# Performance work log

Measured on AMD Instinct MI355X. Metric: run time of the kernel, lower is better.

## Reference

```python
import jax, jax.numpy as jnp
import numpy as np
import math

B, C, F, W = 2, 8, 512, 1024
HEADS = 8


def _mcl(x, Wm, b):
    # per-channel linear over feature dim: x (b,c,g,w), Wm (c,f,g), b (c,f)
    return jnp.einsum('bcgw,cfg->bcfw', x, Wm) + b[None, :, :, None]


def _conv(x, w, b, pad):
    y = jax.lax.conv_general_dilated(
        x, w, window_strides=(1, 1), padding=[(0, 0), (pad, pad)],
        dimension_numbers=('NCHW', 'OIHW', 'NCHW'))
    return y + b[None, :, None, None]


def _rope(t):
    # t: (..., seq, d); lucidrains-style interleaved rotary
    d = t.shape[-1]
    seq = t.shape[-2]
    inv_freq = 1.0 / (10000.0 ** (jnp.arange(0, d, 2, dtype=jnp.float32) / d))
    freqs = jnp.arange(seq, dtype=jnp.float32)[:, None] * inv_freq[None, :]  # (seq, d/2)
    emb = jnp.repeat(freqs, 2, axis=-1)  # (seq, d), interleaved f0,f0,f1,f1,...
    cos, sin = jnp.cos(emb), jnp.sin(emb)
    tp = t.reshape(t.shape[:-1] + (d // 2, 2))
    rot = jnp.stack([-tp[..., 1], tp[..., 0]], axis=-1).reshape(t.shape)
    return t * cos.astype(t.dtype) + rot * sin.astype(t.dtype)


def setup_inputs() -> dict:
    key = jax.random.key(0)
    ks = jax.random.split(key, 18)
    s = 0.02
    d = {'x': jax.random.normal(ks[0], (B, C, F, W), dtype=jnp.float32)}
    names = ['q', 'k', 'v', 'o']
    for i, n in enumerate(names):
        d['W' + n] = jax.random.normal(ks[1 + 4 * i], (C, F, F), dtype=jnp.float32) * s
        d['b' + n] = jnp.zeros((C, F), dtype=jnp.float32)
        kw = 7 if n != 'o' else 1
        d[n + '_conv_w'] = jax.random.normal(ks[2 + 4 * i], (C, C, 1, kw), dtype=jnp.float32) * s
        d[n + '_conv_b'] = jnp.zeros((C,), dtype=jnp.float32)
    return d


def reference(x, Wq, bq, q_conv_w, q_conv_b, Wk, bk, k_conv_w, k_conv_b,
              Wv, bv, v_conv_w, v_conv_b, Wo, bo, o_conv_w, o_conv_b):
    b, c, h, w = x.shape
    dh = h // HEADS

    def split_heads(y):  # (b,c,h,w) -> (b,c,heads,w,dh)
        return y.transpose(0, 1, 3, 2).reshape(b, c, w, HEADS, dh).transpose(0, 1, 3, 2, 4)

    q = _rope(split_heads(_conv(_mcl(x, Wq, bq), q_conv_w, q_conv_b, 3)))
    k = _rope(split_heads(_conv(_mcl(x, Wk, bk), k_conv_w, k_conv_b, 3)))
    v = split_heads(_conv(_mcl(x, Wv, bv), v_conv_w, v_conv_b, 3))

    # forced fp32 attention, scaled by sqrt(h) = sqrt(features)
    qk = jnp.einsum('bceqd,bcekd->bceqk', q.astype(jnp.float32), k.astype(jnp.float32)) / math.sqrt(h)
    a = jax.nn.softmax(qk, axis=-1)
    o = jnp.einsum('bceqk,bcekd->bceqd', a, v.astype(jnp.float32))  # (b,c,heads,w,dh)
    o = o.transpose(0, 1, 3, 2, 4).reshape(b, c, w, h).transpose(0, 1, 3, 2)  # (b,c,h,w)

    return _conv(_mcl(o, Wo, bo), o_conv_w, o_conv_b, 0)
```

## Files before the change

### kernel.cpp

```cpp
#include <hip/hip_runtime.h>
#include <hip/hip_bf16.h>
#include <math.h>

#define W_ 1024
#define F_ 512
#define C_ 8
#define B_ 2
#define DH_ 64

typedef __attribute__((ext_vector_type(8))) short short8;
typedef __attribute__((ext_vector_type(4))) short short4v;
typedef __attribute__((ext_vector_type(4))) float f32x4;

__device__ inline unsigned short f2bf(float x) {
    union { float f; unsigned u; } v; v.f = x;
    unsigned r = v.u + 0x7fff + ((v.u >> 16) & 1);
    return (unsigned short)(r >> 16);
}
__device__ inline float bf2f(unsigned short x) {
    union { unsigned u; float f; } v; v.u = (unsigned)x << 16; return v.f;
}

__device__ inline void gll16(const void* g, void* l) {
    __builtin_amdgcn_global_load_lds(
        (const __attribute__((address_space(1))) unsigned int*)g,
        (__attribute__((address_space(3))) unsigned int*)l, 16, 0, 0);
}

__global__ __launch_bounds__(256) void rope_table_kernel(float* __restrict__ cost,
                                                         float* __restrict__ sint) {
    int idx = blockIdx.x * 256 + threadIdx.x;
    if (idx >= W_ * 32) return;
    int w = idx >> 5, i = idx & 31;
    double freq = pow(10000.0, -(double)(2 * i) / 64.0);
    double ang = (double)w * freq;
    cost[idx] = (float)cos(ang);
    sint[idx] = (float)sin(ang);
}

__global__ __launch_bounds__(256) void xt_kernel(
    const float* __restrict__ In, unsigned short* __restrict__ Out)
{
    const int wt = blockIdx.x;
    const int gc = blockIdx.y;
    const int bc = blockIdx.z;
    __shared__ unsigned short T[128][72];
    const int t = threadIdx.x;
    const float* src = In + (size_t)bc * F_ * W_ + (size_t)gc * 64 * W_ + wt * 128;
    const int d0 = (t >> 4) * 4;
    const int w0 = (t & 15) * 4;
    #pragma unroll
    for (int it = 0; it < 2; ++it) {
        int wbase = w0 + it * 64;
        float4 row[4];
        #pragma unroll
        for (int k = 0; k < 4; ++k)
            row[k] = *(const float4*)(src + (size_t)(d0 + k) * W_ + wbase);
        #pragma unroll
        for (int wp = 0; wp < 4; ++wp) {
            ushort4 p;
            p.x = f2bf(((const float*)&row[0])[wp]);
            p.y = f2bf(((const float*)&row[1])[wp]);
            p.z = f2bf(((const float*)&row[2])[wp]);
            p.w = f2bf(((const float*)&row[3])[wp]);
            *(ushort4*)&T[wbase + wp][d0] = p;
        }
    }
    __syncthreads();
    unsigned short* dst = Out + (size_t)bc * W_ * F_ + (size_t)(wt * 128) * F_ + gc * 64;
    const int w = t >> 1, hf = (t & 1) * 32;
    const unsigned short* sr = &T[w][hf];
    uint4* dr = (uint4*)(dst + (size_t)w * F_ + hf);
    dr[0] = ((const uint4*)sr)[0];
    dr[1] = ((const uint4*)sr)[1];
    dr[2] = ((const uint4*)sr)[2];
    dr[3] = ((const uint4*)sr)[3];
}

template<int BF16OUT>
__device__ inline void mcl_body(const unsigned short* Ag, const unsigned short* Bg,
                                const float* biasp, float* Cp, unsigned short* CpB,
                                int f0, int w0)
{
    __shared__ unsigned short As_[128 * 64];
    __shared__ unsigned short Bs_[128 * 64];
    __shared__ float scr[4][16 * 17];

    const int t = threadIdx.x;
    const int wid = t >> 6, lane = t & 63;
    const int l15 = lane & 15, l4 = lane >> 4;
    const int wf = wid >> 1, ww = wid & 1;

    const int grow = lane >> 3;
    const int gcol = ((lane & 7) * 16) ^ ((grow & 7) << 4);

    f32x4 acc[4][4];
    #pragma unroll
    for (int mt = 0; mt < 4; ++mt)
        #pragma unroll
        for (int nt = 0; nt < 4; ++nt) acc[mt][nt] = (f32x4){0.f, 0.f, 0.f, 0.f};

    for (int ks = 0; ks < 8; ++ks) {
        const int k0 = ks * 64;
        __syncthreads();
        #pragma unroll
        for (int i = 0; i < 4; ++i) {
            int rbase = wid * 32 + i * 8;
            int row = rbase + grow;
            gll16(Ag + (size_t)(f0 + row) * F_ + k0 + (gcol >> 1), &As_[rbase * 64]);
            gll16(Bg + (size_t)(w0 + row) * F_ + k0 + (gcol >> 1), &Bs_[rbase * 64]);
        }
        __syncthreads();
        #pragma unroll
        for (int kf = 0; kf < 2; ++kf) {
            short8 af[4], bf_[4];
            #pragma unroll
            for (int mt = 0; mt < 4; ++mt) {
                int row = wf * 64 + mt * 16 + l15;
                int off = (kf * 64 + l4 * 16) ^ ((row & 7) << 4);
                af[mt] = *(const short8*)((const char*)As_ + row * 128 + off);
            }
            #pragma unroll
            for (int nt = 0; nt < 4; ++nt) {
                int row = ww * 64 + nt * 16 + l15;
                int off = (kf * 64 + l4 * 16) ^ ((row & 7) << 4);
                bf_[nt] = *(const short8*)((const char*)Bs_ + row * 128 + off);
            }
            #pragma unroll
            for (int mt = 0; mt < 4; ++mt)
                #pragma unroll
                for (int nt = 0; nt < 4; ++nt)
                    acc[mt][nt] = __builtin_amdgcn_mfma_f32_16x16x32_bf16(af[mt], bf_[nt], acc[mt][nt], 0, 0, 0);
        }
    }

    const float* bp = biasp + f0 + wf * 64;
    float bz[4][4];
    #pragma unroll
    for (int mt = 0; mt < 4; ++mt)
        #pragma unroll
        for (int r = 0; r < 4; ++r) bz[mt][r] = bp[mt * 16 + l4 * 4 + r];

    float* sw = scr[wid];
    #pragma unroll
    for (int mt = 0; mt < 4; ++mt)
        #pragma unroll
        for (int nt = 0; nt < 4; ++nt) {
            #pragma unroll
            for (int r = 0; r < 4; ++r)
                sw[(l4 * 4 + r) * 17 + l15] = acc[mt][nt][r] + bz[mt][r];
            float4 o;
            o.x = sw[l15 * 17 + l4 * 4 + 0];
            o.y = sw[l15 * 17 + l4 * 4 + 1];
            o.z = sw[l15 * 17 + l4 * 4 + 2];
            o.w = sw[l15 * 17 + l4 * 4 + 3];
            size_t off = (size_t)(f0 + wf * 64 + mt * 16 + l15) * W_
                       + w0 + ww * 64 + nt * 16 + l4 * 4;
            if (BF16OUT) {
                ushort4 p;
                p.x = f2bf(o.x); p.y = f2bf(o.y); p.z = f2bf(o.z); p.w = f2bf(o.w);
                *(ushort4*)(CpB + off) = p;
            } else {
                *(float4*)(Cp + off) = o;
            }
        }
}

__global__ __launch_bounds__(256) void mcl_qkv_kernel(
    const unsigned short* __restrict__ Xt,
    const unsigned short* __restrict__ W0, const unsigned short* __restrict__ W1,
    const unsigned short* __restrict__ W2,
    const float* __restrict__ b0, const float* __restrict__ b1, const float* __restrict__ b2,
    unsigned short* __restrict__ Y0, unsigned short* __restrict__ Y1,
    unsigned short* __restrict__ Y2)
{
    const int zz = blockIdx.z;
    const int proj = zz >> 4, bc = zz & 15;
    const int c = bc & 7;
    const unsigned short* Wb = proj == 0 ? W0 : (proj == 1 ? W1 : W2);
    const float* bias = proj == 0 ? b0 : (proj == 1 ? b1 : b2);
    unsigned short* Y = proj == 0 ? Y0 : (proj == 1 ? Y1 : Y2);
    mcl_body<1>(Wb + (size_t)c * F_ * F_, Xt + (size_t)bc * W_ * F_,
                bias + c * F_, nullptr, Y + (size_t)bc * F_ * W_,
                blockIdx.y * 128, blockIdx.x * 128);
}

__global__ __launch_bounds__(256) void mcl_mfma_kernel(
    const unsigned short* __restrict__ Xt, const unsigned short* __restrict__ Wb,
    const float* __restrict__ bias, float* __restrict__ Y)
{
    const int bc = blockIdx.z;
    const int c = bc & 7;
    mcl_body<0>(Wb + (size_t)c * F_ * F_, Xt + (size_t)bc * W_ * F_,
                bias + c * F_, Y + (size_t)bc * F_ * W_, nullptr,
                blockIdx.y * 128, blockIdx.x * 128);
}

__global__ __launch_bounds__(256) void convrope_w2_kernel(
    const unsigned short* __restrict__ Aq, const unsigned short* __restrict__ Ak,
    const unsigned short* __restrict__ Av,
    unsigned short* __restrict__ Cq, unsigned short* __restrict__ Ck,
    unsigned short* __restrict__ Vb,
    const float* __restrict__ cwq, const float* __restrict__ cbq,
    const float* __restrict__ cwk, const float* __restrict__ cbk,
    const float* __restrict__ cwv, const float* __restrict__ cbv,
    const float* __restrict__ cost, const float* __restrict__ sint)
{
    const int wc = blockIdx.x;
    const int fp = blockIdx.y;
    const int proj = blockIdx.z >> 1;
    const int b = blockIdx.z & 1;
    const unsigned short* In = proj == 0 ? Aq : (proj == 1 ? Ak : Av);
    unsigned short* Out = proj == 0 ? Cq : (proj == 1 ? Ck : Vb);
    const float* CW = proj == 0 ? cwq : (proj == 1 ? cwk : cwv);
    const float* CB = proj == 0 ? cbq : (proj == 1 ? cbk : cbv);
    const int do_rope = (proj < 2);

    __shared__ unsigned rows[C_][264];
    __shared__ float wT[C_][7][C_];
    const int t = threadIdx.x;
    const int w0 = wc * 256;

    #pragma unroll
    for (int ci = 0; ci < 8; ++ci) {
        const unsigned short* s0 = In + ((size_t)(b * C_ + ci) * F_ + 2 * fp) * W_;
        int gw = w0 + t - 3;
        unsigned v = 0;
        if ((unsigned)gw < (unsigned)W_)
            v = (unsigned)s0[gw] | ((unsigned)s0[W_ + gw] << 16);
        rows[ci][t] = v;
        if (t < 8) {
            int gw2 = w0 + 256 + t - 3;
            unsigned v2 = 0;
            if ((unsigned)gw2 < (unsigned)W_)
                v2 = (unsigned)s0[gw2] | ((unsigned)s0[W_ + gw2] << 16);
            rows[ci][256 + t] = v2;
        }
    }
    for (int idx = t; idx < C_ * C_ * 7; idx += 256) {
        int co = idx & 7; int tmp = idx >> 3; int tt = tmp % 7; int ci = tmp / 7;
        wT[ci][tt][co] = CW[((size_t)co * C_ + ci) * 7 + tt];
    }
    float cb[8];
    #pragma unroll
    for (int co = 0; co < 8; co++) cb[co] = CB[co];
    __syncthreads();

    float acc0[8], acc1[8];
    #pragma unroll
    for (int co = 0; co < 8; ++co) { acc0[co] = cb[co]; acc1[co] = cb[co]; }

    #pragma unroll 1
    for (int ci = 0; ci < 8; ++ci) {
        #pragma unroll
        for (int tt = 0; tt < 7; ++tt) {
            float wv[8];
            *(float4*)(wv)     = *(const float4*)&wT[ci][tt][0];
            *(float4*)(wv + 4) = *(const float4*)&wT[ci][tt][4];
            unsigned pv = rows[ci][t + tt];
            union { unsigned u; float f; } c0, c1;
            c0.u = pv << 16;
            c1.u = pv & 0xffff0000u;
            #pragma unroll
            for (int co = 0; co < 8; ++co) {
                acc0[co] = fmaf(c0.f, wv[co], acc0[co]);
                acc1[co] = fmaf(c1.f, wv[co], acc1[co]);
            }
        }
    }

    const int ip = fp & 31;
    const int w = w0 + t;
    float c_ = 1.f, s_ = 0.f;
    if (do_rope) { c_ = cost[w * 32 + ip]; s_ = sint[w * 32 + ip]; }
    #pragma unroll
    for (int co = 0; co < 8; ++co) {
        float o0 = acc0[co], o1 = acc1[co];
        float r0 = do_rope ? (o0 * c_ - o1 * s_) : o0;
        float r1 = do_rope ? (o1 * c_ + o0 * s_) : o1;
        size_t rowb = ((size_t)(b * C_ + co) * F_ + 2 * fp) * W_;
        Out[rowb + w] = f2bf(r0);
        Out[rowb + W_ + w] = f2bf(r1);
    }
}

__global__ __launch_bounds__(256) void transpose_qk_kernel(
    const unsigned short* __restrict__ In, unsigned short* __restrict__ Out, float scale)
{
    const int wt = blockIdx.x;
    const int h = blockIdx.y;
    __shared__ unsigned short T[128][72];
    const int t = threadIdx.x;
    const unsigned short* src = In + (size_t)h * 64 * 1024 + wt * 128;
    const int d0 = (t >> 4) * 4;
    const int w0 = (t & 15) * 4;
    #pragma unroll
    for (int it = 0; it < 2; ++it) {
        int wbase = w0 + it * 64;
        ushort4 row[4];
        #pragma unroll
        for (int k = 0; k < 4; ++k)
            row[k] = *(const ushort4*)(src + (size_t)(d0 + k) * 1024 + wbase);
        #pragma unroll
        for (int wp = 0; wp < 4; ++wp) {
            ushort4 p;
            p.x = f2bf(bf2f(((const unsigned short*)&row[0])[wp]) * scale);
            p.y = f2bf(bf2f(((const unsigned short*)&row[1])[wp]) * scale);
            p.z = f2bf(bf2f(((const unsigned short*)&row[2])[wp]) * scale);
            p.w = f2bf(bf2f(((const unsigned short*)&row[3])[wp]) * scale);
            *(ushort4*)&T[wbase + wp][d0] = p;
        }
    }
    __syncthreads();
    unsigned short* dst = Out + ((size_t)h * 1024 + wt * 128) * 64;
    const int w = t >> 1, hf = (t & 1) * 32;
    const unsigned short* sr = &T[w][hf];
    uint4* dr = (uint4*)(dst + w * 64 + hf);
    dr[0] = ((const uint4*)sr)[0];
    dr[1] = ((const uint4*)sr)[1];
    dr[2] = ((const uint4*)sr)[2];
    dr[3] = ((const uint4*)sr)[3];
}

__global__ __launch_bounds__(256) void bf16cvt_kernel(
    const float* __restrict__ In, unsigned short* __restrict__ Out)
{
    size_t i = ((size_t)blockIdx.x * 256 + threadIdx.x) * 8;
    float4 a = *(const float4*)(In + i);
    float4 b = *(const float4*)(In + i + 4);
    ushort4 pa, pb;
    pa.x = f2bf(a.x); pa.y = f2bf(a.y); pa.z = f2bf(a.z); pa.w = f2bf(a.w);
    pb.x = f2bf(b.x); pb.y = f2bf(b.y); pb.z = f2bf(b.z); pb.w = f2bf(b.w);
    *(ushort4*)(Out + i) = pa;
    *(ushort4*)(Out + i + 4) = pb;
}

__global__ __launch_bounds__(256) void attn_mfma_kernel(
    const unsigned short* __restrict__ Qt, const unsigned short* __restrict__ Kt,
    const unsigned short* __restrict__ Vb, unsigned short* __restrict__ Ot)
{
    const int head = blockIdx.x;
    const int qt = blockIdx.y;
    const int t = threadIdx.x;
    const int wid = t >> 6;
    const int lane = t & 63;
    const int l15 = lane & 15;
    const int l4 = lane >> 4;

    __shared__ unsigned short Ks[64 * 64];
    __shared__ unsigned short Vs[64 * 64];
    __shared__ char plds_[4][11264];
    unsigned short* plds = (unsigned short*)plds_[wid];
    float* olds = (float*)plds_[wid];

    const int q0 = qt * 256 + wid * 64;
    const unsigned short* qb = Qt + ((size_t)head * 1024 + q0) * 64;
    const unsigned short* kb = Kt + (size_t)head * 1024 * 64;
    const unsigned short* vb = Vb + (size_t)head * 64 * 1024;

    short8 aq[4][2];
    #pragma unroll
    for (int mt = 0; mt < 4; ++mt)
        #pragma unroll
        for (int kf = 0; kf < 2; ++kf)
            aq[mt][kf] = *(const short8*)(qb + (size_t)(mt * 16 + l15) * 64 + kf * 32 + l4 * 8);

    const int srow = lane >> 3;
    const int schunk = lane & 7;

    f32x4 oa[4][4];
    float li[4] = {0.f, 0.f, 0.f, 0.f};
    #pragma unroll
    for (int mt = 0; mt < 4; ++mt)
        #pragma unroll
        for (int dt = 0; dt < 4; ++dt) oa[mt][dt] = (f32x4){0.f, 0.f, 0.f, 0.f};

    for (int jt = 0; jt < 16; ++jt) {
        const int j0 = jt * 64;
        __syncthreads();
        #pragma unroll
        for (int i = 0; i < 2; ++i) {
            int rbase = wid * 16 + i * 8;
            int row = rbase + srow;
            gll16(kb + (size_t)(j0 + row) * 64 + ((schunk ^ (row & 7)) * 8), &Ks[rbase * 64]);
            gll16(vb + (size_t)row * 1024 + j0 + ((schunk ^ (row & 7)) * 8), &Vs[rbase * 64]);
        }
        __syncthreads();

        #pragma unroll
        for (int nt = 0; nt < 4; ++nt) {
            int row = nt * 16 + l15;
            short8 bk0 = *(const short8*)&Ks[row * 64 + ((l4 ^ (row & 7)) * 8)];
            short8 bk1 = *(const short8*)&Ks[row * 64 + (((4 + l4) ^ (row & 7)) * 8)];
            #pragma unroll
            for (int mt = 0; mt < 4; ++mt) {
                f32x4 a0 = (f32x4){0.f, 0.f, 0.f, 0.f};
                a0 = __builtin_amdgcn_mfma_f32_16x16x32_bf16(bk0, aq[mt][0], a0, 0, 0, 0);
                a0 = __builtin_amdgcn_mfma_f32_16x16x32_bf16(bk1, aq[mt][1], a0, 0, 0, 0);
                float p0 = __builtin_exp2f(a0[0]);
                float p1 = __builtin_exp2f(a0[1]);
                float p2 = __builtin_exp2f(a0[2]);
                float p3 = __builtin_exp2f(a0[3]);
                li[mt] += (p0 + p1) + (p2 + p3);
                union { __hip_bfloat162 h2[2]; short4v s4; } pk;
                pk.h2[0] = __float22bfloat162_rn(make_float2(p0, p1));
                pk.h2[1] = __float22bfloat162_rn(make_float2(p2, p3));
                *(short4v*)(plds + (size_t)(mt * 16 + l15) * 88 + nt * 16 + l4 * 4) = pk.s4;
            }
        }
        short8 pa[4][2];
        #pragma unroll
        for (int mt = 0; mt < 4; ++mt)
            #pragma unroll
            for (int kf = 0; kf < 2; ++kf)
                pa[mt][kf] = *(const short8*)(plds + (size_t)(mt * 16 + l15) * 88 + kf * 32 + l4 * 8);
        #pragma unroll
        for (int dt = 0; dt < 4; ++dt) {
            int row = dt * 16 + l15;
            short8 bv0 = *(const short8*)&Vs[row * 64 + ((l4 ^ (row & 7)) * 8)];
            short8 bv1 = *(const short8*)&Vs[row * 64 + (((4 + l4) ^ (row & 7)) * 8)];
            #pragma unroll
            for (int mt = 0; mt < 4; ++mt) {
                oa[mt][dt] = __builtin_amdgcn_mfma_f32_16x16x32_bf16(pa[mt][0], bv0, oa[mt][dt], 0, 0, 0);
                oa[mt][dt] = __builtin_amdgcn_mfma_f32_16x16x32_bf16(pa[mt][1], bv1, oa[mt][dt], 0, 0, 0);
            }
        }
    }

    float invq[4][4];
    #pragma unroll
    for (int mt = 0; mt < 4; ++mt) {
        float l = li[mt];
        l += __shfl_xor(l, 16);
        l += __shfl_xor(l, 32);
        float inv = 1.f / l;
        #pragma unroll
        for (int r = 0; r < 4; ++r)
            invq[mt][r] = __shfl(inv, l4 * 4 + r);
    }

    #pragma unroll
    for (int mt = 0; mt < 4; ++mt) {
        #pragma unroll
        for (int dt = 0; dt < 4; ++dt)
            #pragma unroll
            for (int r = 0; r < 4; ++r)
                olds[(size_t)(l4 * 4 + r) * 68 + dt * 16 + l15] = oa[mt][dt][r] * invq[mt][r];
        const int ql = lane >> 2, hf = (lane & 3) * 16;
        const float* srow_ = olds + (size_t)ql * 68 + hf;
        unsigned short* dst = Ot + ((size_t)(head >> 3) * W_ + q0 + mt * 16 + ql) * F_
                                 + (head & 7) * 64 + hf;
        short8 pk0, pk1;
        #pragma unroll
        for (int e = 0; e < 8; ++e) { pk0[e] = (short)f2bf(srow_[e]); pk1[e] = (short)f2bf(srow_[8 + e]); }
        *(short8*)(dst) = pk0;
        *(short8*)(dst + 8) = pk1;
    }
}

__global__ __launch_bounds__(256) void oconv_kernel(
    const float* __restrict__ In, const float* __restrict__ OW,
    const float* __restrict__ OB, float* __restrict__ Out)
{
    size_t idx = (size_t)blockIdx.x * 256 + threadIdx.x;
    int b = (int)(idx >> 19);
    size_t fw = idx & (((size_t)1 << 19) - 1);
    const float* in = In + (size_t)b * C_ * F_ * W_ + fw;
    float* out = Out + (size_t)b * C_ * F_ * W_ + fw;
    float v[8];
    #pragma unroll
    for (int ci = 0; ci < 8; ci++) v[ci] = in[(size_t)ci * F_ * W_];
    #pragma unroll
    for (int co = 0; co < 8; co++) {
        float acc = OB[co];
        #pragma unroll
        for (int ci = 0; ci < 8; ci++) acc = fmaf(v[ci], OW[co * 8 + ci], acc);
        out[(size_t)co * F_ * W_] = acc;
    }
}

extern "C" void kernel_launch(void* const* d_in, const int* in_sizes, int n_in,
                              void* d_out, int out_size, void* d_ws, size_t ws_size,
                              hipStream_t stream) {
    const float* x   = (const float*)d_in[0];
    const float* Wq  = (const float*)d_in[1];
    const float* bq  = (const float*)d_in[2];
    const float* qcw = (const float*)d_in[3];
    const float* qcb = (const float*)d_in[4];
    const float* Wk  = (const float*)d_in[5];
    const float* bk  = (const float*)d_in[6];
    const float* kcw = (const float*)d_in[7];
    const float* kcb = (const float*)d_in[8];
    const float* Wv  = (const float*)d_in[9];
    const float* bv  = (const float*)d_in[10];
    const float* vcw = (const float*)d_in[11];
    const float* vcb = (const float*)d_in[12];
    const float* Wo  = (const float*)d_in[13];
    const float* bo  = (const float*)d_in[14];
    const float* ocw = (const float*)d_in[15];
    const float* ocb = (const float*)d_in[16];

    float* ws = (float*)d_ws;
    const size_t SZ = (size_t)B_ * C_ * F_ * W_;
    const size_t WSF = (size_t)C_ * F_ * F_ / 2;
    unsigned short* Aq = (unsigned short*)ws;
    unsigned short* Cq = Aq + SZ;
    unsigned short* Ak = (unsigned short*)(ws + SZ);
    unsigned short* Ck = Ak + SZ;
    unsigned short* Av = (unsigned short*)(ws + 2 * SZ);
    unsigned short* XtVb = (unsigned short*)(ws + 3 * SZ);
    unsigned short* WqB = (unsigned short*)(ws + 3 * SZ + SZ / 2);
    unsigned short* WkB = (unsigned short*)(ws + 3 * SZ + SZ / 2 + 2 * WSF);
    unsigned short* WvB = (unsigned short*)(ws + 3 * SZ + SZ / 2 + 4 * WSF);
    unsigned short* WoB = (unsigned short*)(ws + 3 * SZ + SZ / 2 + 6 * WSF);
    unsigned short* Qt  = (unsigned short*)(ws + 2 * SZ);
    unsigned short* Kt  = Qt + SZ;
    unsigned short* Ot  = (unsigned short*)ws;
    float* Ao = ws + SZ;
    float* cost = ws + 4 * SZ;
    float* sint = cost + (size_t)W_ * 32;

    const float qscale = (float)(1.4426950408889634 / 22.627416997969522);

    rope_table_kernel<<<(W_ * 32 + 255) / 256, 256, 0, stream>>>(cost, sint);
    xt_kernel<<<dim3(8, 8, 16), 256, 0, stream>>>(x, XtVb);
    bf16cvt_kernel<<<1024, 256, 0, stream>>>(Wq, WqB);
    bf16cvt_kernel<<<1024, 256, 0, stream>>>(Wk, WkB);
    bf16cvt_kernel<<<1024, 256, 0, stream>>>(Wv, WvB);
    bf16cvt_kernel<<<1024, 256, 0, stream>>>(Wo, WoB);

    mcl_qkv_kernel<<<dim3(8, 4, 48), 256, 0, stream>>>(
        XtVb, WqB, WkB, WvB, bq, bk, bv, Aq, Ak, Av);

    convrope_w2_kernel<<<dim3(4, F_ / 2, 6), 256, 0, stream>>>(
        Aq, Ak, Av, Cq, Ck, XtVb,
        qcw, qcb, kcw, kcb, vcw, vcb, cost, sint);

    transpose_qk_kernel<<<dim3(W_ / 128, 128), 256, 0, stream>>>(Cq, Qt, qscale);
    transpose_qk_kernel<<<dim3(W_ / 128, 128), 256, 0, stream>>>(Ck, Kt, 1.0f);

    attn_mfma_kernel<<<dim3(128, 4), 256, 0, stream>>>(Qt, Kt, XtVb, Ot);

    mcl_mfma_kernel<<<dim3(8, 4, 16), 256, 0, stream>>>(Ot, WoB, bo, Ao);
    oconv_kernel<<<(B_ * F_ * W_) / 256, 256, 0, stream>>>(Ao, ocw, ocb, (float*)d_out);
}
```

Measured before the change: 247.6 us.

## Double-buffer K/V tiles and process P in half-tiles to cut LDS

K and V tiles in shared memory now use two buffers. The next tile is prefetched with global_load_lds while the current one is being computed, which removes one of the two barriers per iteration. The softmax-probability staging buffer is also split into two 32-column halves, so each half feeds the PV MFMAs right away and the per-wave P buffer shrinks. This should hide global load latency, and the smaller P buffer offsets the extra LDS taken by the second K/V buffer. The catch is that correctness depends on the async loads having completed at the single barrier, and the epilogue's reuse of the smaller per-wave buffer must still fit.

```diff
diff --git a/kernel.cpp b/kernel.cpp
--- a/kernel.cpp
+++ b/kernel.cpp
@@ -347,9 +347,9 @@
     const int l15 = lane & 15;
     const int l4 = lane >> 4;
 
-    __shared__ unsigned short Ks[64 * 64];
-    __shared__ unsigned short Vs[64 * 64];
-    __shared__ char plds_[4][11264];
+    __shared__ unsigned short Ks[2][64 * 64];
+    __shared__ unsigned short Vs[2][64 * 64];
+    __shared__ char plds_[4][5120];
     unsigned short* plds = (unsigned short*)plds_[wid];
     float* olds = (float*)plds_[wid];
 
@@ -375,54 +375,67 @@
         #pragma unroll
         for (int dt = 0; dt < 4; ++dt) oa[mt][dt] = (f32x4){0.f, 0.f, 0.f, 0.f};
 
+    #pragma unroll
+    for (int i = 0; i < 2; ++i) {
+        int rbase = wid * 16 + i * 8;
+        int row = rbase + srow;
+        gll16(kb + (size_t)row * 64 + ((schunk ^ (row & 7)) * 8), &Ks[0][rbase * 64]);
+        gll16(vb + (size_t)row * 1024 + ((schunk ^ (row & 7)) * 8), &Vs[0][rbase * 64]);
+    }
+
     for (int jt = 0; jt < 16; ++jt) {
-        const int j0 = jt * 64;
+        const int cur = jt & 1;
         __syncthreads();
-        #pragma unroll
-        for (int i = 0; i < 2; ++i) {
-            int rbase = wid * 16 + i * 8;
-            int row = rbase + srow;
-            gll16(kb + (size_t)(j0 + row) * 64 + ((schunk ^ (row & 7)) * 8), &Ks[rbase * 64]);
-            gll16(vb + (size_t)row * 1024 + j0 + ((schunk ^ (row & 7)) * 8), &Vs[rbase * 64]);
-        }
-        __syncthreads();
-
-        #pragma unroll
-        for (int nt = 0; nt < 4; ++nt) {
-            int row = nt * 16 + l15;
-            short8 bk0 = *(const short8*)&Ks[row * 64 + ((l4 ^ (row & 7)) * 8)];
-            short8 bk1 = *(const short8*)&Ks[row * 64 + (((4 + l4) ^ (row & 7)) * 8)];
-            #pragma unroll
-            for (int mt = 0; mt < 4; ++mt) {
-                f32x4 a0 = (f32x4){0.f, 0.f, 0.f, 0.f};
-                a0 = __builtin_amdgcn_mfma_f32_16x16x32_bf16(bk0, aq[mt][0], a0, 0, 0, 0);
-                a0 = __builtin_amdgcn_mfma_f32_16x16x32_bf16(bk1, aq[mt][1], a0, 0, 0, 0);
-                float p0 = __builtin_exp2f(a0[0]);
-                float p1 = __builtin_exp2f(a0[1]);
-                float p2 = __builtin_exp2f(a0[2]);
-                float p3 = __builtin_exp2f(a0[3]);
-                li[mt] += (p0 + p1) + (p2 + p3);
-                union { __hip_bfloat162 h2[2]; short4v s4; } pk;
-                pk.h2[0] = __float22bfloat162_rn(make_float2(p0, p1));
-                pk.h2[1] = __float22bfloat162_rn(make_float2(p2, p3));
-                *(short4v*)(plds + (size_t)(mt * 16 + l15) * 88 + nt * 16 + l4 * 4) = pk.s4;
-            }
-        }
-        short8 pa[4][2];
-        #pragma unroll
-        for (int mt = 0; mt < 4; ++mt)
-            #pragma unroll
-            for (int kf = 0; kf < 2; ++kf)
-                pa[mt][kf] = *(const short8*)(plds + (size_t)(mt * 16 + l15) * 88 + kf * 32 + l4 * 8);
-        #pragma unroll
-        for (int dt = 0; dt < 4; ++dt) {
-            int row = dt * 16 + l15;
-            short8 bv0 = *(const short8*)&Vs[row * 64 + ((l4 ^ (row & 7)) * 8)];
-            short8 bv1 = *(const short8*)&Vs[row * 64 + (((4 + l4) ^ (row & 7)) * 8)];
-            #pragma unroll
-            for (int mt = 0; mt < 4; ++mt) {
-                oa[mt][dt] = __builtin_amdgcn_mfma_f32_16x16x32_bf16(pa[mt][0], bv0, oa[mt][dt], 0, 0, 0);
-                oa[mt][dt] = __builtin_amdgcn_mfma_f32_16x16x32_bf16(pa[mt][1], bv1, oa[mt][dt], 0, 0, 0);
+        if (jt < 15) {
+            const int j1 = (jt + 1) * 64;
+            #pragma unroll
+            for (int i = 0; i < 2; ++i) {
+                int rbase = wid * 16 + i * 8;
+                int row = rbase + srow;
+                gll16(kb + (size_t)(j1 + row) * 64 + ((schunk ^ (row & 7)) * 8),
+                      &Ks[cur ^ 1][rbase * 64]);
+                gll16(vb + (size_t)row * 1024 + j1 + ((schunk ^ (row & 7)) * 8),
+                      &Vs[cur ^ 1][rbase * 64]);
+            }
+        }
+        const unsigned short* Kc = Ks[cur];
+        const unsigned short* Vc = Vs[cur];
+
+        #pragma unroll
+        for (int jh = 0; jh < 2; ++jh) {
+            #pragma unroll
+            for (int nt2 = 0; nt2 < 2; ++nt2) {
+                int nt = jh * 2 + nt2;
+                int row = nt * 16 + l15;
+                short8 bk0 = *(const short8*)&Kc[row * 64 + ((l4 ^ (row & 7)) * 8)];
+                short8 bk1 = *(const short8*)&Kc[row * 64 + (((4 + l4) ^ (row & 7)) * 8)];
+                #pragma unroll
+                for (int mt = 0; mt < 4; ++mt) {
+                    f32x4 a0 = (f32x4){0.f, 0.f, 0.f, 0.f};
+                    a0 = __builtin_amdgcn_mfma_f32_16x16x32_bf16(bk0, aq[mt][0], a0, 0, 0, 0);
+                    a0 = __builtin_amdgcn_mfma_f32_16x16x32_bf16(bk1, aq[mt][1], a0, 0, 0, 0);
+                    float p0 = __builtin_exp2f(a0[0]);
+                    float p1 = __builtin_exp2f(a0[1]);
+                    float p2 = __builtin_exp2f(a0[2]);
+                    float p3 = __builtin_exp2f(a0[3]);
+                    li[mt] += (p0 + p1) + (p2 + p3);
+                    union { __hip_bfloat162 h2[2]; short4v s4; } pk;
+                    pk.h2[0] = __float22bfloat162_rn(make_float2(p0, p1));
+                    pk.h2[1] = __float22bfloat162_rn(make_float2(p2, p3));
+                    *(short4v*)(plds + (size_t)(mt * 16 + l15) * 40 + nt2 * 16 + l4 * 4) = pk.s4;
+                }
+            }
+            short8 pa[4];
+            #pragma unroll
+            for (int mt = 0; mt < 4; ++mt)
+                pa[mt] = *(const short8*)(plds + (size_t)(mt * 16 + l15) * 40 + l4 * 8);
+            #pragma unroll
+            for (int dt = 0; dt < 4; ++dt) {
+                int row = dt * 16 + l15;
+                short8 bv = *(const short8*)&Vc[row * 64 + (((jh * 4 + l4) ^ (row & 7)) * 8)];
+                #pragma unroll
+                for (int mt = 0; mt < 4; ++mt)
+                    oa[mt][dt] = __builtin_amdgcn_mfma_f32_16x16x32_bf16(pa[mt], bv, oa[mt][dt], 0, 0, 0);
             }
         }
     }
```

Measured after the change: 248.4 us. No clear change (+0.3%).

## Software-pipeline attention PV with next QK tile and fuse weight conversions

Applied to the files above, without the earlier changes.

The attention loop now double-buffers the V tile and defers each tile's P·V MFMAs into the next iteration, interleaving them with the current tile's Q·K MFMAs and exp work. The goal is to hide exp and LDS latency behind matrix work, with one final P·V pass after the loop. The per-wave P buffer stride drops from 88 to 68 elements to shrink LDS, which may cause misaligned 16-byte LDS reads or bank conflicts. The four separate weight-to-bf16 conversion launches are also merged into one launch indexed by blockIdx.y, saving launch overhead.

```diff
diff --git a/kernel.cpp b/kernel.cpp
--- a/kernel.cpp
+++ b/kernel.cpp
@@ -322,15 +322,21 @@
     dr[3] = ((const uint4*)sr)[3];
 }
 
-__global__ __launch_bounds__(256) void bf16cvt_kernel(
-    const float* __restrict__ In, unsigned short* __restrict__ Out)
-{
+__global__ __launch_bounds__(256) void wcvt4_kernel(
+    const float* __restrict__ S0, const float* __restrict__ S1,
+    const float* __restrict__ S2, const float* __restrict__ S3,
+    unsigned short* __restrict__ D0, unsigned short* __restrict__ D1,
+    unsigned short* __restrict__ D2, unsigned short* __restrict__ D3)
+{
+    const int a = blockIdx.y;
+    const float* In = a == 0 ? S0 : (a == 1 ? S1 : (a == 2 ? S2 : S3));
+    unsigned short* Out = a == 0 ? D0 : (a == 1 ? D1 : (a == 2 ? D2 : D3));
     size_t i = ((size_t)blockIdx.x * 256 + threadIdx.x) * 8;
-    float4 a = *(const float4*)(In + i);
-    float4 b = *(const float4*)(In + i + 4);
+    float4 va = *(const float4*)(In + i);
+    float4 vb = *(const float4*)(In + i + 4);
     ushort4 pa, pb;
-    pa.x = f2bf(a.x); pa.y = f2bf(a.y); pa.z = f2bf(a.z); pa.w = f2bf(a.w);
-    pb.x = f2bf(b.x); pb.y = f2bf(b.y); pb.z = f2bf(b.z); pb.w = f2bf(b.w);
+    pa.x = f2bf(va.x); pa.y = f2bf(va.y); pa.z = f2bf(va.z); pa.w = f2bf(va.w);
+    pb.x = f2bf(vb.x); pb.y = f2bf(vb.y); pb.z = f2bf(vb.z); pb.w = f2bf(vb.w);
     *(ushort4*)(Out + i) = pa;
     *(ushort4*)(Out + i + 4) = pb;
 }
@@ -348,8 +354,8 @@
     const int l4 = lane >> 4;
 
     __shared__ unsigned short Ks[64 * 64];
-    __shared__ unsigned short Vs[64 * 64];
-    __shared__ char plds_[4][11264];
+    __shared__ unsigned short Vs[2][64 * 64];
+    __shared__ char plds_[4][8704];
     unsigned short* plds = (unsigned short*)plds_[wid];
     float* olds = (float*)plds_[wid];
 
@@ -376,6 +382,7 @@
         for (int dt = 0; dt < 4; ++dt) oa[mt][dt] = (f32x4){0.f, 0.f, 0.f, 0.f};
 
     for (int jt = 0; jt < 16; ++jt) {
+        const int cur = jt & 1;
         const int j0 = jt * 64;
         __syncthreads();
         #pragma unroll
@@ -383,42 +390,68 @@
             int rbase = wid * 16 + i * 8;
             int row = rbase + srow;
             gll16(kb + (size_t)(j0 + row) * 64 + ((schunk ^ (row & 7)) * 8), &Ks[rbase * 64]);
-            gll16(vb + (size_t)row * 1024 + j0 + ((schunk ^ (row & 7)) * 8), &Vs[rbase * 64]);
+            gll16(vb + (size_t)row * 1024 + j0 + ((schunk ^ (row & 7)) * 8), &Vs[cur][rbase * 64]);
         }
         __syncthreads();
+
+        short8 pa[4][2];
+        if (jt > 0) {
+            #pragma unroll
+            for (int mt = 0; mt < 4; ++mt)
+                #pragma unroll
+                for (int kf = 0; kf < 2; ++kf)
+                    pa[mt][kf] = *(const short8*)(plds + (size_t)(mt * 16 + l15) * 68 + kf * 32 + l4 * 8);
+        }
 
         #pragma unroll
         for (int nt = 0; nt < 4; ++nt) {
             int row = nt * 16 + l15;
             short8 bk0 = *(const short8*)&Ks[row * 64 + ((l4 ^ (row & 7)) * 8)];
             short8 bk1 = *(const short8*)&Ks[row * 64 + (((4 + l4) ^ (row & 7)) * 8)];
+            f32x4 s[4];
             #pragma unroll
             for (int mt = 0; mt < 4; ++mt) {
                 f32x4 a0 = (f32x4){0.f, 0.f, 0.f, 0.f};
                 a0 = __builtin_amdgcn_mfma_f32_16x16x32_bf16(bk0, aq[mt][0], a0, 0, 0, 0);
                 a0 = __builtin_amdgcn_mfma_f32_16x16x32_bf16(bk1, aq[mt][1], a0, 0, 0, 0);
-                float p0 = __builtin_exp2f(a0[0]);
-                float p1 = __builtin_exp2f(a0[1]);
-                float p2 = __builtin_exp2f(a0[2]);
-                float p3 = __builtin_exp2f(a0[3]);
+                s[mt] = a0;
+            }
+            if (jt > 0) {
+                short8 bv0 = *(const short8*)&Vs[cur ^ 1][row * 64 + ((l4 ^ (row & 7)) * 8)];
+                short8 bv1 = *(const short8*)&Vs[cur ^ 1][row * 64 + (((4 + l4) ^ (row & 7)) * 8)];
+                #pragma unroll
+                for (int mt = 0; mt < 4; ++mt) {
+                    oa[mt][nt] = __builtin_amdgcn_mfma_f32_16x16x32_bf16(pa[mt][0], bv0, oa[mt][nt], 0, 0, 0);
+                    oa[mt][nt] = __builtin_amdgcn_mfma_f32_16x16x32_bf16(pa[mt][1], bv1, oa[mt][nt], 0, 0, 0);
+                }
+            }
+            #pragma unroll
+            for (int mt = 0; mt < 4; ++mt) {
+                float p0 = __builtin_exp2f(s[mt][0]);
+                float p1 = __builtin_exp2f(s[mt][1]);
+                float p2 = __builtin_exp2f(s[mt][2]);
+                float p3 = __builtin_exp2f(s[mt][3]);
                 li[mt] += (p0 + p1) + (p2 + p3);
                 union { __hip_bfloat162 h2[2]; short4v s4; } pk;
                 pk.h2[0] = __float22bfloat162_rn(make_float2(p0, p1));
                 pk.h2[1] = __float22bfloat162_rn(make_float2(p2, p3));
-                *(short4v*)(plds + (size_t)(mt * 16 + l15) * 88 + nt * 16 + l4 * 4) = pk.s4;
-            }
-        }
+                *(short4v*)(plds + (size_t)(mt * 16 + l15) * 68 + nt * 16 + l4 * 4) = pk.s4;
+            }
+        }
+    }
+
+    {
         short8 pa[4][2];
         #pragma unroll
         for (int mt = 0; mt < 4; ++mt)
             #pragma unroll
             for (int kf = 0; kf < 2; ++kf)
-                pa[mt][kf] = *(const short8*)(plds + (size_t)(mt * 16 + l15) * 88 + kf * 32 + l4 * 8);
+                pa[mt][kf] = *(const short8*)(plds + (size_t)(mt * 16 + l15) * 68 + kf * 32 + l4 * 8);
         #pragma unroll
         for (int dt = 0; dt < 4; ++dt) {
             int row = dt * 16 + l15;
-            short8 bv0 = *(const short8*)&Vs[row * 64 + ((l4 ^ (row & 7)) * 8)];
-            short8 bv1 = *(const short8*)&Vs[row * 64 + (((4 + l4) ^ (row & 7)) * 8)];
+            short8 bv0 = *(const short8*)&Vs[1][row * 64 + ((l4 ^ (row & 7)) * 8)];
+            short8 bv1 = *(const short8*)&Vs[1][row * 64 + (((4 + l4) ^ (row & 7)) * 8)];
             #pragma unroll
             for (int mt = 0; mt < 4; ++mt) {
                 oa[mt][dt] = __builtin_amdgcn_mfma_f32_16x16x32_bf16(pa[mt][0], bv0, oa[mt][dt], 0, 0, 0);
@@ -524,10 +557,7 @@
 
     rope_table_kernel<<<(W_ * 32 + 255) / 256, 256, 0, stream>>>(cost, sint);
     xt_kernel<<<dim3(8, 8, 16), 256, 0, stream>>>(x, XtVb);
-    bf16cvt_kernel<<<1024, 256, 0, stream>>>(Wq, WqB);
-    bf16cvt_kernel<<<1024, 256, 0, stream>>>(Wk, WkB);
-    bf16cvt_kernel<<<1024, 256, 0, stream>>>(Wv, WvB);
-    bf16cvt_kernel<<<1024, 256, 0, stream>>>(Wo, WoB);
+    wcvt4_kernel<<<dim3(1024, 4), 256, 0, stream>>>(Wq, Wk, Wv, Wo, WqB, WkB, WvB, WoB);
 
     mcl_qkv_kernel<<<dim3(8, 4, 48), 256, 0, stream>>>(
         XtVb, WqB, WkB, WvB, bq, bk, bv, Aq, Ak, Av);
```

New measurement: 260.3 us. 5.1% more time.
